# Optimization experiments

Measured on AMD Instinct MI355X. Metric: run time of the kernel, lower is better.

Reference implementation:

```python
import jax, jax.numpy as jnp
import numpy as np

B, S, D, H = 2, 2048, 1024, 16
DK = D // H

def setup_inputs() -> dict:
    key = jax.random.key(0)
    ks = jax.random.split(key, 8)
    def lin(k):
        kw, kb = jax.random.split(k)
        w = jax.random.normal(kw, (D, D), dtype=jnp.float32) / np.sqrt(D)
        b = jax.random.normal(kb, (D,), dtype=jnp.float32) * 0.01
        return w, b
    wq, bq = lin(ks[0]); wk, bk = lin(ks[1]); wv, bv = lin(ks[2]); wo, bo = lin(ks[3])
    return {
        'q': jax.random.normal(ks[4], (B, S, D), dtype=jnp.float32),
        'k': jax.random.normal(ks[5], (B, S, D), dtype=jnp.float32),
        'v': jax.random.normal(ks[6], (B, S, D), dtype=jnp.float32),
        'mask': jnp.ones((1, 1, S, S), dtype=jnp.int32),
        'wq': wq, 'bq': bq, 'wk': wk, 'bk': bk,
        'wv': wv, 'bv': bv, 'wo': wo, 'bo': bo,
    }

def reference(q, k, v, mask, wq, bq, wk, bk, wv, bv, wo, bo):
    b, s, _ = q.shape
    # QKV projections (nn.Linear: x @ W^T + b)
    Q = (q @ wq.T + bq).reshape(b, s, H, DK).transpose(0, 2, 1, 3)  # [B,H,S,DK]
    K = (k @ wk.T + bk).reshape(b, -1, H, DK).transpose(0, 2, 1, 3)
    V = (v @ wv.T + bv).reshape(b, -1, H, DK).transpose(0, 2, 1, 3)
    scores = jnp.einsum('bhqd,bhkd->bhqk', Q, K) / np.sqrt(DK)
    # faithful to source: masked positions set to -1e-09 (tiny, as written)
    scores = jnp.where(mask == 0, jnp.float32(-1e-09), scores)
    att = jax.nn.softmax(scores, axis=-1)
    x = jnp.einsum('bhqk,bhkd->bhqd', att, V)
    x = x.transpose(0, 2, 1, 3).reshape(b, s, H * DK)
    return x @ wo.T + bo
```

## Files before the change

### kernel.cpp

```cpp
#include <hip/hip_runtime.h>
#include <stdint.h>

typedef unsigned short u16;
typedef unsigned int u32;
typedef __bf16 bf16x8 __attribute__((ext_vector_type(8)));
typedef __bf16 bf16x2 __attribute__((ext_vector_type(2)));
typedef float f32x4 __attribute__((ext_vector_type(4)));
typedef float f32x16 __attribute__((ext_vector_type(16)));
typedef unsigned short u16x4 __attribute__((ext_vector_type(4)));
typedef unsigned short u16x8 __attribute__((ext_vector_type(8)));
typedef u32 u32x4 __attribute__((ext_vector_type(4)));

#define B_ 2
#define S_ 2048
#define D_ 1024
#define H_ 16

__device__ __forceinline__ u16 f2bf(float f) {
  uint32_t u = __builtin_bit_cast(uint32_t, f);
  u += 0x7FFF + ((u >> 16) & 1);
  return (u16)(u >> 16);
}

__device__ __forceinline__ u32 pkbf(float x, float y) {
  bf16x2 t;
  t.x = (__bf16)x;
  t.y = (__bf16)y;
  return __builtin_bit_cast(u32, t);
}

__device__ __forceinline__ void pl32swap(u32& a, u32& b) {
  asm("v_permlane32_swap_b32 %0, %1" : "+v"(a), "+v"(b));
}

__device__ __forceinline__ float max3f(float a, float b, float c) {
  return fmaxf(fmaxf(a, b), c);
}

__device__ __forceinline__ void gld_lds16(const void* g, void* l) {
  __builtin_amdgcn_global_load_lds((const __attribute__((address_space(1))) void*)g,
                                   (__attribute__((address_space(3))) void*)l, 16, 0, 0);
}

__global__ void cvt_w3(const float* __restrict__ wq, const float* __restrict__ wk,
                       const float* __restrict__ wv, u16* __restrict__ wqb,
                       u16* __restrict__ wkb, u16* __restrict__ wvb) {
  int bid = blockIdx.x;
  const float* s;
  u16* d;
  int base;
  if (bid < 1024)       { s = wq; d = wqb; base = bid; }
  else if (bid < 2048)  { s = wk; d = wkb; base = bid - 1024; }
  else                  { s = wv; d = wvb; base = bid - 2048; }
  int i = (base * 256 + threadIdx.x) * 4;
  float4 f = *(const float4*)(s + i);
  u16x4 o;
  o.x = f2bf(f.x); o.y = f2bf(f.y); o.z = f2bf(f.z); o.w = f2bf(f.w);
  *(u16x4*)(d + i) = o;
}

template <int EPI, bool A_FP32, int BN>
__device__ __forceinline__ void gemm_body(const void* __restrict__ Ap, const u16* __restrict__ W,
                                          const float* __restrict__ bias, void* __restrict__ Cp,
                                          float scale, int m0, int n0) {
  constexpr int K = 1024;
  constexpr int N = 1024;
  constexpr int NFR = BN / 32;
  __shared__ __align__(16) u16 As[128 * 64];
  __shared__ __align__(16) u16 Ws[BN * 64];
  const int tid = threadIdx.x;
  const int lane = tid & 63, wid = tid >> 6;
  const int wm = wid >> 1, wn = wid & 1;
  const int l15 = lane & 15, l4 = lane >> 4;

  f32x4 acc[4][NFR] = {};

  float4 areg[8];
  auto loadA = [&](int kt) {
    if (A_FP32) {
      const float* Af = (const float*)Ap;
#pragma unroll
      for (int i = 0; i < 4; ++i) {
        int c = i * 256 + tid;
        int row = c >> 3, col8 = c & 7;
        const float* src = Af + (size_t)(m0 + row) * K + kt * 64 + col8 * 8;
        areg[2 * i]     = *(const float4*)(src);
        areg[2 * i + 1] = *(const float4*)(src + 4);
      }
    }
  };
  auto writeA = [&]() {
#pragma unroll
    for (int i = 0; i < 4; ++i) {
      int c = i * 256 + tid;
      int row = c >> 3, col8 = c & 7;
      u16x8 o;
      o[0] = f2bf(areg[2 * i].x);     o[1] = f2bf(areg[2 * i].y);
      o[2] = f2bf(areg[2 * i].z);     o[3] = f2bf(areg[2 * i].w);
      o[4] = f2bf(areg[2 * i + 1].x); o[5] = f2bf(areg[2 * i + 1].y);
      o[6] = f2bf(areg[2 * i + 1].z); o[7] = f2bf(areg[2 * i + 1].w);
      *(u16x8*)((char*)As + row * 128 + ((col8 << 4) ^ ((row & 7) << 4))) = o;
    }
  };

  loadA(0);
  for (int kt = 0; kt < K / 64; ++kt) {
    __syncthreads();
    if (A_FP32) {
      writeA();
    } else {
      const u16* Ab = (const u16*)Ap;
#pragma unroll
      for (int i = 0; i < 4; ++i) {
        int c = i * 256 + tid;
        int row = c >> 3;
        int scb = ((c & 7) << 4) ^ ((row & 7) << 4);
        gld_lds16(Ab + (size_t)(m0 + row) * K + (size_t)kt * 64 + (scb >> 1),
                  (char*)As + (size_t)c * 16);
      }
    }
#pragma unroll
    for (int i = 0; i < BN / 32; ++i) {
      int c = i * 256 + tid;
      int row = c >> 3;
      int scb = ((c & 7) << 4) ^ ((row & 7) << 4);
      gld_lds16(W + (size_t)(n0 + row) * K + (size_t)kt * 64 + (scb >> 1),
                (char*)Ws + (size_t)c * 16);
    }
    if (A_FP32 && kt + 1 < K / 64) loadA(kt + 1);
    __syncthreads();
#pragma unroll
    for (int kk = 0; kk < 2; ++kk) {
      bf16x8 af[4], bfr[NFR];
#pragma unroll
      for (int m = 0; m < 4; ++m) {
        int row = wm * 64 + m * 16 + l15;
        int cb = (kk * 64 + l4 * 16) ^ ((row & 7) << 4);
        af[m] = *(const bf16x8*)((const char*)As + row * 128 + cb);
      }
#pragma unroll
      for (int n = 0; n < NFR; ++n) {
        int row = wn * (BN / 2) + n * 16 + l15;
        int cb = (kk * 64 + l4 * 16) ^ ((row & 7) << 4);
        bfr[n] = *(const bf16x8*)((const char*)Ws + row * 128 + cb);
      }
#pragma unroll
      for (int m = 0; m < 4; ++m)
#pragma unroll
        for (int n = 0; n < NFR; ++n)
          acc[m][n] = __builtin_amdgcn_mfma_f32_16x16x32_bf16(af[m], bfr[n], acc[m][n], 0, 0, 0);
    }
  }

  if (EPI == 0) {
    float* C = (float*)Cp;
#pragma unroll
    for (int m = 0; m < 4; ++m)
#pragma unroll
      for (int n = 0; n < NFR; ++n) {
        int col = n0 + wn * (BN / 2) + n * 16 + l15;
        float bval = bias[col];
#pragma unroll
        for (int j = 0; j < 4; ++j) {
          int r = m0 + wm * 64 + m * 16 + l4 * 4 + j;
          C[(size_t)r * N + col] = acc[m][n][j] + bval;
        }
      }
  } else if (EPI == 1) {
    u16* C = (u16*)Cp;
#pragma unroll
    for (int m = 0; m < 4; ++m)
#pragma unroll
      for (int n = 0; n < NFR; ++n) {
        int col = n0 + wn * (BN / 2) + n * 16 + l15;
        float bval = bias[col];
        int h = col >> 6, dk = col & 63;
#pragma unroll
        for (int j = 0; j < 4; ++j) {
          int r = m0 + wm * 64 + m * 16 + l4 * 4 + j;
          int bb = r >> 11, s = r & 2047;
          C[(((size_t)bb * H_ + h) * S_ + s) * 64 + dk] = f2bf((acc[m][n][j] + bval) * scale);
        }
      }
  } else {
    u16* C = (u16*)Cp;
#pragma unroll
    for (int m = 0; m < 4; ++m)
#pragma unroll
      for (int n = 0; n < NFR; ++n) {
        int col = n0 + wn * (BN / 2) + n * 16 + l15;
        float bval = bias[col];
        int h = col >> 6, dk = col & 63;
        int r0 = m0 + wm * 64 + m * 16 + l4 * 4;
        int bb = r0 >> 11, s0 = r0 & 2047;
        u16x4 o;
#pragma unroll
        for (int j = 0; j < 4; ++j) o[j] = f2bf(acc[m][n][j] + bval);
        *(u16x4*)(C + (((size_t)bb * H_ + h) * 64 + dk) * S_ + s0) = o;
      }
  }
}

__global__ __launch_bounds__(256) void gemm_qkv(
    const float* __restrict__ q, const float* __restrict__ k, const float* __restrict__ v,
    const u16* __restrict__ wqb, const u16* __restrict__ wkb, const u16* __restrict__ wvb,
    const float* __restrict__ bq, const float* __restrict__ bk, const float* __restrict__ bv,
    u16* __restrict__ Qp, u16* __restrict__ Kp, u16* __restrict__ VTp) {
  const int flat = blockIdx.x;
  const int nf = (flat & 7) * 96 + (flat >> 3);
  const int zz = nf >> 8, rem = nf & 255;
  const int n0 = (rem & 7) * 128, m0 = (rem >> 3) * 128;
  if (zz == 2) {
    gemm_body<2, true, 128>(v, wvb, bv, VTp, 1.0f, m0, n0);
  } else if (zz == 1) {
    gemm_body<1, true, 128>(k, wkb, bk, Kp, 1.0f, m0, n0);
  } else {
    gemm_body<1, true, 128>(q, wqb, bq, Qp, 0.1803368801111244f, m0, n0);
  }
}

__global__ __launch_bounds__(256) void gemm_out(
    const u16* __restrict__ xb, const u16* __restrict__ wob,
    const float* __restrict__ bo, float* __restrict__ out) {
  const int flat = blockIdx.x;
  const int nf = (flat & 7) * 64 + (flat >> 3);
  const int n0 = (nf & 15) * 64, m0 = (nf >> 4) * 128;
  gemm_body<0, false, 64>(xb, wob, bo, out, 1.0f, m0, n0);
}

__global__ __launch_bounds__(256, 2) void attn(
    const u16* __restrict__ Qp, const u16* __restrict__ Kp,
    const u16* __restrict__ VTp, u16* __restrict__ xb,
    const float* __restrict__ wo, u16* __restrict__ wob) {
  if (blockIdx.x >= 512) {
    int base = (int)(blockIdx.x - 512) * 4096 + threadIdx.x * 4;
#pragma unroll
    for (int j = 0; j < 4; ++j) {
      int i = base + j * 1024;
      float4 f = *(const float4*)(wo + i);
      u16x4 o;
      o.x = f2bf(f.x); o.y = f2bf(f.y); o.z = f2bf(f.z); o.w = f2bf(f.w);
      *(u16x4*)(wob + i) = o;
    }
    return;
  }

  const int flat = blockIdx.x;
  const int nf = (flat & 7) * 64 + (flat >> 3);
  const int bh = nf >> 4, qt = nf & 15;
  const int b = bh >> 4, h = bh & 15;
  const size_t kbase = (size_t)bh * S_ * 64;
  const int tid = threadIdx.x, lane = tid & 63, w = tid >> 6;
  const int l31 = lane & 31, hi = lane >> 5;

  __shared__ __align__(16) u16 Ks[2][64 * 64];
  __shared__ __align__(16) u16 Vs[3][64 * 64];

  bf16x8 qf[4];
  {
    const u16* qrow = Qp + kbase + (size_t)(qt * 128 + w * 32 + l31) * 64;
#pragma unroll
    for (int kk = 0; kk < 4; ++kk)
      qf[kk] = *(const bf16x8*)(qrow + kk * 16 + hi * 8);
  }

  float m = -1e30f, lsum = 0.f;
  f32x16 xacc[2] = {};
  bf16x8 pf[4];

  auto stageK = [&](int bi, int t) {
#pragma unroll
    for (int i = 0; i < 2; ++i) {
      int c = i * 256 + tid;
      int row = c >> 3;
      int scb = (((c & 7) ^ (row & 7) ^ ((row >> 3) & 3)) << 4);
      gld_lds16(Kp + kbase + (size_t)(t * 64 + row) * 64 + (scb >> 1),
                (char*)Ks[bi] + (size_t)c * 16);
    }
  };
  auto stageV = [&](int bi, int t) {
#pragma unroll
    for (int i = 0; i < 2; ++i) {
      int c = i * 256 + tid;
      int row = c >> 3;
      int scb = (((c & 7) ^ (row & 7) ^ ((row >> 3) & 3)) << 4);
      gld_lds16(VTp + kbase + (size_t)row * S_ + t * 64 + (scb >> 1),
                (char*)Vs[bi] + (size_t)c * 16);
    }
  };

  auto pv = [&](const u16* Vb) {
    __builtin_amdgcn_s_setprio(1);
#pragma unroll
    for (int kk = 0; kk < 4; ++kk)
#pragma unroll
      for (int dn = 0; dn < 2; ++dn) {
        int row = dn * 32 + l31;
        int cb = (kk * 32 + hi * 16) ^ ((((row & 7) ^ ((row >> 3) & 3))) << 4);
        bf16x8 vf = *(const bf16x8*)((const char*)Vb + row * 128 + cb);
        xacc[dn] = __builtin_amdgcn_mfma_f32_32x32x16_bf16(pf[kk], vf, xacc[dn], 0, 0, 0);
      }
    __builtin_amdgcn_s_setprio(0);
  };

  int vprev = 2, vcur = 0, vnext = 1;
  stageK(0, 0);
  stageV(0, 0);
  for (int t = 0; t < S_ / 64; ++t) {
    __syncthreads();
    if (t + 1 < S_ / 64) {
      stageK((t + 1) & 1, t + 1);
      stageV(vnext, t + 1);
    }

    const u16* Kb = Ks[t & 1];

    f32x16 sacc[2] = {};
    __builtin_amdgcn_s_setprio(1);
#pragma unroll
    for (int kk = 0; kk < 4; ++kk)
#pragma unroll
      for (int kvt = 0; kvt < 2; ++kvt) {
        int row = kvt * 32 + l31;
        int cb = (kk * 32 + hi * 16) ^ ((((row & 7) ^ ((row >> 3) & 3))) << 4);
        bf16x8 kf = *(const bf16x8*)((const char*)Kb + row * 128 + cb);
        sacc[kvt] = __builtin_amdgcn_mfma_f32_32x32x16_bf16(kf, qf[kk], sacc[kvt], 0, 0, 0);
      }
    __builtin_amdgcn_s_setprio(0);

    if (t) pv(Vs[vprev]);

    float mx;
    {
      float t0 = max3f(sacc[0][0], sacc[0][1], sacc[0][2]);
      float t1 = max3f(sacc[0][3], sacc[0][4], sacc[0][5]);
      float t2 = max3f(sacc[0][6], sacc[0][7], sacc[0][8]);
      float t3 = max3f(sacc[0][9], sacc[0][10], sacc[0][11]);
      float t4 = max3f(sacc[0][12], sacc[0][13], sacc[0][14]);
      float t5 = max3f(sacc[0][15], sacc[1][0], sacc[1][1]);
      float t6 = max3f(sacc[1][2], sacc[1][3], sacc[1][4]);
      float t7 = max3f(sacc[1][5], sacc[1][6], sacc[1][7]);
      float t8 = max3f(sacc[1][8], sacc[1][9], sacc[1][10]);
      float t9 = max3f(sacc[1][11], sacc[1][12], sacc[1][13]);
      float ta = fmaxf(sacc[1][14], sacc[1][15]);
      float u0 = max3f(t0, t1, t2);
      float u1 = max3f(t3, t4, t5);
      float u2 = max3f(t6, t7, t8);
      float u3 = fmaxf(t9, ta);
      float x = fmaxf(max3f(u0, u1, u2), u3);
      mx = fmaxf(x, __shfl_xor(x, 32, 64));
    }

    if (__any(mx - m > 8.f)) {
      float nm = fmaxf(m, mx);
      float sc = __builtin_amdgcn_exp2f(m - nm);
      m = nm;
      lsum *= sc;
#pragma unroll
      for (int r = 0; r < 16; ++r) {
        int src = ((r & 3) + 8 * (r >> 2) + 4 * hi) | (hi << 5);
        float f = __shfl(sc, src, 64);
        xacc[0][r] *= f;
        xacc[1][r] *= f;
      }
    }

    float p[2][16];
    float sum = 0.f;
#pragma unroll
    for (int t2 = 0; t2 < 2; ++t2)
#pragma unroll
      for (int r = 0; r < 16; ++r) {
        float e = __builtin_amdgcn_exp2f(sacc[t2][r] - m);
        p[t2][r] = e;
        sum += e;
      }
    sum += __shfl_xor(sum, 32, 64);
    lsum += sum;

#pragma unroll
    for (int kk = 0; kk < 4; ++kk) {
      const int t2 = kk >> 1, rb = (kk & 1) * 8;
      u32 a0 = pkbf(p[t2][rb + 0], p[t2][rb + 1]);
      u32 a1 = pkbf(p[t2][rb + 2], p[t2][rb + 3]);
      u32 b0 = pkbf(p[t2][rb + 4], p[t2][rb + 5]);
      u32 b1 = pkbf(p[t2][rb + 6], p[t2][rb + 7]);
      pl32swap(a0, b0);
      pl32swap(a1, b1);
      u32x4 wv;
      wv.x = a0; wv.y = a1; wv.z = b0; wv.w = b1;
      pf[kk] = __builtin_bit_cast(bf16x8, wv);
    }

    vprev = vcur; vcur = vnext; vnext = (vnext + 1 == 3) ? 0 : vnext + 1;
  }

  pv(Vs[vprev]);

  float linv = 1.f / lsum;
#pragma unroll
  for (int r = 0; r < 16; ++r) {
    int qr = (r & 3) + 8 * (r >> 2) + 4 * hi;
    float f = __shfl(linv, qr | (hi << 5), 64);
    int qg = qt * 128 + w * 32 + qr;
    size_t rowb = ((size_t)b * S_ + qg) * D_ + h * 64;
    xb[rowb + l31] = f2bf(xacc[0][r] * f);
    xb[rowb + 32 + l31] = f2bf(xacc[1][r] * f);
  }
}

extern "C" void kernel_launch(void* const* d_in, const int* in_sizes, int n_in,
                              void* d_out, int out_size, void* d_ws, size_t ws_size,
                              hipStream_t stream) {
  const float* q  = (const float*)d_in[0];
  const float* k  = (const float*)d_in[1];
  const float* v  = (const float*)d_in[2];
  const float* wq = (const float*)d_in[4];
  const float* bq = (const float*)d_in[5];
  const float* wk = (const float*)d_in[6];
  const float* bk = (const float*)d_in[7];
  const float* wv = (const float*)d_in[8];
  const float* bv = (const float*)d_in[9];
  const float* wo = (const float*)d_in[10];
  const float* bo = (const float*)d_in[11];
  float* out = (float*)d_out;

  char* ws = (char*)d_ws;
  const size_t MB = 1u << 20;
  u16* wqb = (u16*)(ws + 0 * MB);
  u16* wkb = (u16*)(ws + 2 * MB);
  u16* wvb = (u16*)(ws + 4 * MB);
  u16* wob = (u16*)(ws + 6 * MB);
  u16* Qp  = (u16*)(ws + 8 * MB);
  u16* Kp  = (u16*)(ws + 16 * MB);
  u16* VTp = (u16*)(ws + 24 * MB);
  u16* xb  = (u16*)(ws + 32 * MB);

  cvt_w3<<<3072, 256, 0, stream>>>(wq, wk, wv, wqb, wkb, wvb);
  gemm_qkv<<<768, 256, 0, stream>>>(q, k, v, wqb, wkb, wvb,
                                    bq, bk, bv, Qp, Kp, VTp);
  attn<<<768, 256, 0, stream>>>(Qp, Kp, VTp, xb, wo, wob);
  gemm_out<<<512, 256, 0, stream>>>(xb, wob, bo, out);
}
```

Before: 126.0 us.

## Load K and V fragments directly from global memory into registers, dropping LDS staging

Removes the shared-memory double/triple buffering of K and V tiles and the per-iteration block barrier. Each wave now loads its own MFMA operand fragments straight from global memory into registers, issuing the K loads before the deferred PV MFMAs and the V loads after the QK MFMAs. This drops the syncthreads and LDS traffic, but the four waves in a block each fetch the same K/V data, which raises global/L2 traffic, and load latency is no longer hidden by an async prefetch one tile ahead.

```diff
diff --git a/kernel.cpp b/kernel.cpp
--- a/kernel.cpp
+++ b/kernel.cpp
@@ -253,8 +253,8 @@
   const int tid = threadIdx.x, lane = tid & 63, w = tid >> 6;
   const int l31 = lane & 31, hi = lane >> 5;
 
-  __shared__ __align__(16) u16 Ks[2][64 * 64];
-  __shared__ __align__(16) u16 Vs[3][64 * 64];
+  const u16* Kb = Kp + kbase;
+  const u16* Vb = VTp + kbase;
 
   bf16x8 qf[4];
   {
@@ -267,68 +267,46 @@
   float m = -1e30f, lsum = 0.f;
   f32x16 xacc[2] = {};
   bf16x8 pf[4];
-
-  auto stageK = [&](int bi, int t) {
-#pragma unroll
-    for (int i = 0; i < 2; ++i) {
-      int c = i * 256 + tid;
-      int row = c >> 3;
-      int scb = (((c & 7) ^ (row & 7) ^ ((row >> 3) & 3)) << 4);
-      gld_lds16(Kp + kbase + (size_t)(t * 64 + row) * 64 + (scb >> 1),
-                (char*)Ks[bi] + (size_t)c * 16);
-    }
-  };
-  auto stageV = [&](int bi, int t) {
-#pragma unroll
-    for (int i = 0; i < 2; ++i) {
-      int c = i * 256 + tid;
-      int row = c >> 3;
-      int scb = (((c & 7) ^ (row & 7) ^ ((row >> 3) & 3)) << 4);
-      gld_lds16(VTp + kbase + (size_t)row * S_ + t * 64 + (scb >> 1),
-                (char*)Vs[bi] + (size_t)c * 16);
-    }
-  };
-
-  auto pv = [&](const u16* Vb) {
+  bf16x8 vfp[8];
+
+  auto pv = [&]() {
     __builtin_amdgcn_s_setprio(1);
 #pragma unroll
     for (int kk = 0; kk < 4; ++kk)
 #pragma unroll
-      for (int dn = 0; dn < 2; ++dn) {
-        int row = dn * 32 + l31;
-        int cb = (kk * 32 + hi * 16) ^ ((((row & 7) ^ ((row >> 3) & 3))) << 4);
-        bf16x8 vf = *(const bf16x8*)((const char*)Vb + row * 128 + cb);
-        xacc[dn] = __builtin_amdgcn_mfma_f32_32x32x16_bf16(pf[kk], vf, xacc[dn], 0, 0, 0);
-      }
+      for (int dn = 0; dn < 2; ++dn)
+        xacc[dn] = __builtin_amdgcn_mfma_f32_32x32x16_bf16(pf[kk], vfp[kk * 2 + dn],
+                                                           xacc[dn], 0, 0, 0);
     __builtin_amdgcn_s_setprio(0);
   };
 
-  int vprev = 2, vcur = 0, vnext = 1;
-  stageK(0, 0);
-  stageV(0, 0);
   for (int t = 0; t < S_ / 64; ++t) {
-    __syncthreads();
-    if (t + 1 < S_ / 64) {
-      stageK((t + 1) & 1, t + 1);
-      stageV(vnext, t + 1);
-    }
-
-    const u16* Kb = Ks[t & 1];
+    bf16x8 kf[8];
+#pragma unroll
+    for (int kk = 0; kk < 4; ++kk)
+#pragma unroll
+      for (int kvt = 0; kvt < 2; ++kvt)
+        kf[kk * 2 + kvt] = *(const bf16x8*)(
+            Kb + (size_t)(t * 64 + kvt * 32 + l31) * 64 + kk * 16 + hi * 8);
+
+    if (t) pv();
 
     f32x16 sacc[2] = {};
     __builtin_amdgcn_s_setprio(1);
 #pragma unroll
     for (int kk = 0; kk < 4; ++kk)
 #pragma unroll
-      for (int kvt = 0; kvt < 2; ++kvt) {
-        int row = kvt * 32 + l31;
-        int cb = (kk * 32 + hi * 16) ^ ((((row & 7) ^ ((row >> 3) & 3))) << 4);
-        bf16x8 kf = *(const bf16x8*)((const char*)Kb + row * 128 + cb);
-        sacc[kvt] = __builtin_amdgcn_mfma_f32_32x32x16_bf16(kf, qf[kk], sacc[kvt], 0, 0, 0);
-      }
+      for (int kvt = 0; kvt < 2; ++kvt)
+        sacc[kvt] = __builtin_amdgcn_mfma_f32_32x32x16_bf16(kf[kk * 2 + kvt], qf[kk],
+                                                            sacc[kvt], 0, 0, 0);
     __builtin_amdgcn_s_setprio(0);
 
-    if (t) pv(Vs[vprev]);
+#pragma unroll
+    for (int kk = 0; kk < 4; ++kk)
+#pragma unroll
+      for (int dn = 0; dn < 2; ++dn)
+        vfp[kk * 2 + dn] = *(const bf16x8*)(
+            Vb + (size_t)(dn * 32 + l31) * S_ + t * 64 + kk * 16 + hi * 8);
 
     float mx;
     {
@@ -391,11 +369,9 @@
       wv.x = a0; wv.y = a1; wv.z = b0; wv.w = b1;
       pf[kk] = __builtin_bit_cast(bf16x8, wv);
     }
-
-    vprev = vcur; vcur = vnext; vnext = (vnext + 1 == 3) ? 0 : vnext + 1;
-  }
-
-  pv(Vs[vprev]);
+  }
+
+  pv();
 
   float linv = 1.f / lsum;
 #pragma unroll
```

After: 193.7 us. 1.54x slower.
